# Performance work log

Measured on AMD Instinct MI355X. Metric: run time of the kernel, lower is better.

The kernel has to match this reference:

```python
import jax, jax.numpy as jnp
import numpy as np
from jax.scipy.linalg import expm

N_SPINS = 7
DIM = 2 ** N_SPINS  # 128
DT = 1e-05
B0 = 80.0
T2 = 1.0
PHASE = 0.0
SW = 1000.0


def _spin_ops():
    # Build per-spin angular-momentum operators via Kronecker embedding.
    sx = np.array([[0, 1], [1, 0]], dtype=np.complex64) / 2
    sy = np.array([[0, -1j], [1j, 0]], dtype=np.complex64) / 2
    sz = np.array([[1, 0], [0, -1]], dtype=np.complex64) / 2

    def embed(s):
        ops = []
        for i in range(N_SPINS):
            left = np.eye(2 ** i) if i > 0 else np.array(1.0)
            right = np.eye(2 ** (N_SPINS - i - 1)) if N_SPINS - i - 1 > 0 else np.array(1.0)
            ops.append(np.kron(np.kron(left, s), right))
        return np.stack(ops).astype(np.complex64)  # [n_spins, dim, dim]

    return embed(sx), embed(sy), embed(sz)


_IX, _IY, _IZ = _spin_ops()


def setup_inputs() -> dict:
    key = jax.random.key(0)
    h_mat = jax.random.normal(key, (N_SPINS, N_SPINS), dtype=jnp.float32)
    return {"h_mat": h_mat, "n_samp": 4096}


def reference(h_mat, n_samp):
    Ix = jnp.asarray(_IX)  # [n, d, d]
    Iy = jnp.asarray(_IY)
    Iz = jnpp_asarray = jnp.asarray(_IZ)
    Iz = jnp.asarray(_IZ)

    IHy = Iy.sum(axis=0)
    IHz = Iz.sum(axis=0)
    Op = Ix.sum(axis=0) + 1j * IHy  # IHx + i IHy

    hc = h_mat.astype(jnp.complex64)
    two_pi = 2.0 * jnp.pi

    # Pairwise two-spin couplings: C[i,j] = Ix_i Ix_j + Iy_i Iy_j + Iz_i Iz_j
    pair = (jnp.einsum('iab,jbc->ijac', Ix, Ix)
            + jnp.einsum('iab,jbc->ijac', Iy, Iy)
            + jnp.einsum('iab,jbc->ijac', Iz, Iz))
    upper = jnp.triu(jnp.ones((N_SPINS, N_SPINS), dtype=jnp.complex64), k=1)

    H0 = (two_pi * B0 * jnp.einsum('i,iab->ab', jnp.diagonal(hc), Iz)
          + two_pi * jnp.einsum('ij,ijac->ac', hc * upper, pair))

    # 90y pulse, then free evolution propagator
    U90y = expm(-1j * (jnp.pi / 2) * IHy)
    rho0 = U90y @ IHz @ U90y.conj().T
    P = expm(-1j * H0 * DT)
    Pd = P.conj().T

    def step(rho, _):
        tr = jnp.einsum('ij,ji->', Op, rho)  # trace(Op @ rho)
        return P @ rho @ Pd, tr

    _, traces = jax.lax.scan(step, rho0, None, length=n_samp)

    apod = jnp.exp((-DT / T2) * jnp.arange(n_samp, dtype=jnp.float32))
    FID = traces * apod.astype(jnp.complex64)

    spec = jnp.fft.fftshift(jnp.fft.fft(FID, 2 * n_samp))
    FTspec = jnp.exp(jnp.complex64(1j * PHASE)) * spec

    AQ = n_samp / SW
    time_series = jnp.linspace(0.0, AQ, n_samp, dtype=jnp.float32)
    freq_series = jnp.linspace(-SW / 2, SW / 2, 2 * n_samp, dtype=jnp.float32)
    return FID, time_series, FTspec, freq_series
```

## Files before the change

### kernel.cpp

```cpp
#include <hip/hip_runtime.h>
#include <math.h>

#define N_SAMP 4096
#define NS     7
#define DT_F   1e-5f
#define B0_F   80.0f
#define T2_F   1.0f
#define SW_F   1000.0f
#define TWO_PI 6.2831853071795864769f
#define EIG_T  640


__global__ __launch_bounds__(EIG_T) void k_eig(const float* __restrict__ h,
                                               float* __restrict__ Vc,
                                               float* __restrict__ Uc,
                                               float* __restrict__ lam_out) {
    const int nsz_[8]   = {1, 7, 21, 35, 35, 21, 7, 1};
    const int nbase_[8] = {0, 1, 8, 29, 64, 99, 120, 127};
    const int cum2_[8]  = {0, 1, 50, 491, 1716, 2941, 3382, 3431};
    const int offsU_[8] = {0, 0, 7, 154, 889, 2114, 2849, 2996};
    const int s    = blockIdx.x;
    const int ns   = nsz_[s];
    const int base = nbase_[s];
    const int tid  = threadIdx.x;
    const int wave = tid >> 6;
    const int lane = tid & 63;

    __shared__ float As[36 * 37];
    __shared__ float Vs[36 * 37];
    __shared__ int   st[36];
    __shared__ int   stm1[36];
    __shared__ int   inv[128];
    __shared__ float hs[49];
    __shared__ int   ppt2[21 * 12];
    __shared__ int   cnt2[21];

    const int ksm1 = (s >= 1) ? nsz_[s - 1] : 0;

    if (tid < 49) hs[tid] = h[tid];
    if (tid < 21) cnt2[tid] = 0;
    if (tid == 0) {
        int cnt = 0;
        for (int r = 0; r < 128; ++r) if (__popc(r) == s) st[cnt++] = r;
    }
    if (tid == 1 && s >= 1) {
        int cnt = 0;
        for (int r = 0; r < 128; ++r) if (__popc(r) == s - 1) stm1[cnt++] = r;
    }
    if (tid < 128 && __popc(tid) == s) {
        int cnt = 0;
        for (int r = 0; r < 128; ++r) { if (r == tid) break; if (__popc(r) == s) ++cnt; }
        inv[tid] = cnt;
    }
    for (int t = tid; t < 36 * 37; t += EIG_T) { As[t] = 0.f; Vs[t] = 0.f; }
    __syncthreads();

    if (ns > 1) {
        const int off_[7] = {0, 6, 11, 15, 18, 20, 0};
        for (int r = tid; r < 128; r += EIG_T) {
            if (__popc(r) == s) {
                for (int i = 0; i < 6; ++i) {
                    if (!((r >> i) & 1)) continue;
                    for (int j = i + 1; j < 7; ++j) {
                        if ((r >> j) & 1) continue;
                        int rid = off_[i] + (j - i - 1);
                        int prt = r ^ ((1 << i) | (1 << j));
                        int slot = atomicAdd(&cnt2[rid], 1);
                        ppt2[rid * 12 + slot] = (inv[r] << 8) | inv[prt];
                    }
                }
            }
        }
    }

    for (int t = tid; t < ns * ns; t += EIG_T) {
        int i = t / ns, j = t % ns;
        int r = st[i], c = st[j];
        float val = 0.f;
        if (r == c) {
            float acc = 0.f;
            for (int a = 0; a < 7; ++a) {
                float za = ((r >> (6 - a)) & 1) ? -0.5f : 0.5f;
                acc += B0_F * hs[a * 7 + a] * za;
                for (int b = a + 1; b < 7; ++b) {
                    float zb = ((r >> (6 - b)) & 1) ? -0.5f : 0.5f;
                    acc += hs[a * 7 + b] * za * zb;
                }
            }
            val = TWO_PI * acc;
        } else {
            int x = r ^ c;
            if (__popc(x) == 2) {
                int u = 31 - __clz(x);
                int v = __ffs(x) - 1;
                if (((r >> u) & 1) != ((r >> v) & 1))
                    val = TWO_PI * 0.5f * hs[(6 - u) * 7 + (6 - v)];
            }
        }
        As[i * 37 + j] = val;
    }
    for (int i = tid; i < ns; i += EIG_T) Vs[i * 37 + i] = 1.f;
    __syncthreads();

    if (ns > 1) {
        for (int t = 0; t < 21; ++t) {
            int npr = cnt2[t];
            float c0 = 1.f, s0 = 0.f;
            int   pq0 = -1;
            if (wave < npr) {
                int pq = ppt2[t * 12 + wave];
                int p = pq >> 8, q = pq & 255;
                float app = As[p * 37 + p];
                float aqq = As[q * 37 + q];
                float apq = As[p * 37 + q];
                float c = 1.f, sn = 0.f;
                if (fabsf(apq) >= 1e-30f) {
                    float tau = (aqq - app) / (2.f * apq);
                    float tt  = copysignf(1.f / (fabsf(tau) + sqrtf(1.f + tau * tau)), tau);
                    c  = rsqrtf(1.f + tt * tt);
                    sn = tt * c;
                }
                c0 = c; s0 = sn; pq0 = pq;
                if (lane < ns) {
                    float ap = As[p * 37 + lane], aq = As[q * 37 + lane];
                    As[p * 37 + lane] = c * ap - sn * aq;
                    As[q * 37 + lane] = sn * ap + c * aq;
                    float vp = Vs[p * 37 + lane], vq = Vs[q * 37 + lane];
                    Vs[p * 37 + lane] = c * vp - sn * vq;
                    Vs[q * 37 + lane] = sn * vp + c * vq;
                }
            }
            __syncthreads();
            if (pq0 >= 0) {
                int p = pq0 >> 8, q = pq0 & 255;
                if (lane < ns) {
                    float ap = As[lane * 37 + p], aq = As[lane * 37 + q];
                    As[lane * 37 + p] = c0 * ap - s0 * aq;
                    As[lane * 37 + q] = s0 * ap + c0 * aq;
                }
            }
            __syncthreads();
        }
    }

    for (int i = tid; i < ns; i += EIG_T) lam_out[base + i] = As[i * 37 + i];
    for (int t = tid; t < ns * ns; t += EIG_T) {
        int a = t / ns, k = t - (t / ns) * ns;
        Vc[cum2_[s] + t] = Vs[a * 37 + k];
    }
    if (s >= 1) {
        for (int t = tid; t < ns * ksm1; t += EIG_T) {
            int a = t / ksm1, i = t - (t / ksm1) * ksm1;
            int rr = stm1[i];
            float uval = 0.f;
#pragma unroll
            for (int p = 0; p < 7; ++p)
                if (!((rr >> p) & 1)) uval += Vs[a * 37 + inv[rr + (1 << p)]];
            Uc[offsU_[s] + t] = uval;
        }
    }
}

__global__ __launch_bounds__(128) void k_mwc(const float* __restrict__ Vc,
                                             const float* __restrict__ Uc,
                                             float* __restrict__ wc,
                                             int* __restrict__ ab) {
    const int n1_[7]   = {1, 7, 21, 35, 35, 21, 7};
    const int n2_[7]   = {7, 21, 35, 35, 21, 7, 1};
    const int offs_[7] = {0, 7, 154, 889, 2114, 2849, 2996};
    const int nb1_[7]  = {0, 1, 8, 29, 64, 99, 120};
    const int nb2_[7]  = {1, 8, 29, 64, 99, 120, 127};
    const int cum2_[7] = {0, 1, 50, 491, 1716, 2941, 3382};
    int e = blockIdx.x * 128 + threadIdx.x;
    if (e >= 3072) return;
    if (e >= 3003) { wc[e] = 0.f; ab[e] = 0; return; }
    int t = 0;
#pragma unroll
    for (int u = 1; u < 7; ++u) if (e >= offs_[u]) t = u;
    int loc = e - offs_[t];
    int n1 = n1_[t], n2 = n2_[t];
    int i = loc / n2;
    int j = loc - i * n2;
    const float* va = &Vc[cum2_[t] + i * n1];
    const float* ub = &Uc[offs_[t] + j * n1];
    float acc = 0.f;
    for (int k = 0; k < n1; ++k) acc += va[k] * ub[k];
    wc[e] = 0.5f * acc * acc;
    ab[e] = ((nb1_[t] + i) << 7) | (nb2_[t] + j);
}

__global__ __launch_bounds__(256) void k_fid(const float* __restrict__ wc,
                                             const int* __restrict__ ab,
                                             const float* __restrict__ lam,
                                             float* __restrict__ fidfF,
                                             float* __restrict__ out) {
    __shared__ float2 cb0[128], dd[128];
    __shared__ float  lred[4][16];
    const int n0  = blockIdx.x * 8;
    const int tid = threadIdx.x;
    const float t0 = (float)n0 * DT_F;
    if (tid < 128) {
        float sn, cs;
        sincosf(lam[tid] * t0, &sn, &cs);
        cb0[tid] = make_float2(cs, -sn);
        sincosf(lam[tid] * DT_F, &sn, &cs);
        dd[tid] = make_float2(cs, -sn);
    }
    __syncthreads();

    float ar0=0,ar1=0,ar2=0,ar3=0,ar4=0,ar5=0,ar6=0,ar7=0;
    float ai0=0,ai1=0,ai2=0,ai3=0,ai4=0,ai5=0,ai6=0,ai7=0;
#pragma unroll 4
    for (int i = 0; i < 12; ++i) {
        int e = i * 256 + tid;
        float w = wc[e];
        int pq = ab[e];
        int a = pq >> 7, b = pq & 127;
        float2 ca = cb0[a], cbv = cb0[b];
        float2 da = dd[a],  db  = dd[b];
        float zr = ca.x * cbv.x + ca.y * cbv.y;
        float zi = ca.x * cbv.y - ca.y * cbv.x;
        float fr = da.x * db.x + da.y * db.y;
        float fi = da.x * db.y - da.y * db.x;
        ar0 += w * zr; ai0 += w * zi; { float tr = zr*fr - zi*fi; zi = zr*fi + zi*fr; zr = tr; }
        ar1 += w * zr; ai1 += w * zi; { float tr = zr*fr - zi*fi; zi = zr*fi + zi*fr; zr = tr; }
        ar2 += w * zr; ai2 += w * zi; { float tr = zr*fr - zi*fi; zi = zr*fi + zi*fr; zr = tr; }
        ar3 += w * zr; ai3 += w * zi; { float tr = zr*fr - zi*fi; zi = zr*fi + zi*fr; zr = tr; }
        ar4 += w * zr; ai4 += w * zi; { float tr = zr*fr - zi*fi; zi = zr*fi + zi*fr; zr = tr; }
        ar5 += w * zr; ai5 += w * zi; { float tr = zr*fr - zi*fi; zi = zr*fi + zi*fr; zr = tr; }
        ar6 += w * zr; ai6 += w * zi; { float tr = zr*fr - zi*fi; zi = zr*fi + zi*fr; zr = tr; }
        ar7 += w * zr; ai7 += w * zi;
    }

    const int wave = tid >> 6, lane = tid & 63;
    float acc[16] = {ar0,ai0,ar1,ai1,ar2,ai2,ar3,ai3,ar4,ai4,ar5,ai5,ar6,ai6,ar7,ai7};
#pragma unroll 16
    for (int v = 0; v < 16; ++v) {
        float x = acc[v];
        for (int off = 32; off > 0; off >>= 1) x += __shfl_down(x, off);
        if (lane == 0) lred[wave][v] = x;
    }
    __syncthreads();
    if (tid < 16) {
        float x = lred[0][tid] + lred[1][tid] + lred[2][tid] + lred[3][tid];
        int jj = tid >> 1, c = tid & 1;
        int n = n0 + jj;
        float ap = expf(-(DT_F / T2_F) * (float)n);
        x *= ap;
        fidfF[2 * n + c] = x;
        if (c == 0) out[n] = x;
    }
}

__global__ __launch_bounds__(256) void k_dft(const float2* __restrict__ fidf,
                                             float* __restrict__ part) {
    __shared__ float2 fs[256];
    const int tid = threadIdx.x;
    const int ch  = blockIdx.x >> 5;
    const int kb  = blockIdx.x & 31;
    const int n0  = ch * 256;
    fs[tid] = fidf[n0 + tid];
    __syncthreads();
    const int k = kb * 256 + tid;
    const int K = (k + 4096) & 8191;
    const float C = TWO_PI / 8192.0f;
    int idx = (n0 * K) & 8191;
    float ar = 0.f;
    for (int i = 0; i < 256; ++i) {
        float2 s = fs[i];
        float sn, cs;
        __sincosf(C * (float)idx, &sn, &cs);
        ar += s.x * cs + s.y * sn;
        idx = (idx + K) & 8191;
    }
    part[ch * 8192 + k] = ar;
}

__global__ void k_dredax(const float* __restrict__ part, float* __restrict__ out) {
    int i = blockIdx.x * 256 + threadIdx.x;
    float s = 0.f;
#pragma unroll
    for (int ch = 0; ch < 16; ++ch) s += part[ch * 8192 + i];
    out[8192 + i] = s;
    out[16384 + i] = -0.5f * SW_F + (float)i * (SW_F / (float)(2 * N_SAMP - 1));
    if (i < N_SAMP)
        out[4096 + i] = (float)i * ((N_SAMP / SW_F) / (float)(N_SAMP - 1));
}

extern "C" void kernel_launch(void* const* d_in, const int* in_sizes, int n_in,
                              void* d_out, int out_size, void* d_ws, size_t ws_size,
                              hipStream_t stream) {
    const float* h = (const float*)d_in[0];
    float* out = (float*)d_out;
    float* ws  = (float*)d_ws;

    float*  Vc   = ws;
    float*  Uc   = ws + 4096;
    float*  lam  = ws + 16384;
    float*  wc   = ws + 49280;
    int*    ab   = (int*)(ws + 52352);
    float*  fidfF= ws + 65664;
    float2* fidf = (float2*)(ws + 65664);
    float*  part = ws + 73856;

    k_eig<<<8, EIG_T, 0, stream>>>(h, Vc, Uc, lam);
    k_mwc<<<24, 128, 0, stream>>>(Vc, Uc, wc, ab);
    k_fid<<<512, 256, 0, stream>>>(wc, ab, lam, fidfF, out);
    k_dft<<<512, 256, 0, stream>>>(fidf, part);
    k_dredax<<<32, 256, 0, stream>>>(part, out);
}
```

Measured before the change: 61.97 us.

## Compute spectrum analytically from eigen-transitions instead of DFT of FID

Replaces the two-stage DFT over the sampled FID (partial sums plus a reduction kernel) with a closed-form geometric-series sum over the ~3000 transition weights for each frequency bin. k_mwc now also precomputes each transition's half-phase step and its decayed end-phase factor, and k_spec evaluates the complex ratio per bin from shared memory. This removes the FID-to-spectrum dependency and one kernel launch, and cuts the per-bin work from 4096 samples to 3003 transitions. In exchange it relies on a hardcoded apodization constant and per-term divisions that may lose precision near resonances.

Result: slower. 101.7 us (+64.1%).

```diff
diff --git a/kernel.cpp b/kernel.cpp
--- a/kernel.cpp
+++ b/kernel.cpp
@@ -163,8 +163,12 @@
 
 __global__ __launch_bounds__(128) void k_mwc(const float* __restrict__ Vc,
                                              const float* __restrict__ Uc,
+                                             const float* __restrict__ lam,
                                              float* __restrict__ wc,
-                                             int* __restrict__ ab) {
+                                             int* __restrict__ ab,
+                                             float* __restrict__ hl,
+                                             float* __restrict__ sr,
+                                             float* __restrict__ si) {
     const int n1_[7]   = {1, 7, 21, 35, 35, 21, 7};
     const int n2_[7]   = {7, 21, 35, 35, 21, 7, 1};
     const int offs_[7] = {0, 7, 154, 889, 2114, 2849, 2996};
@@ -173,7 +177,7 @@
     const int cum2_[7] = {0, 1, 50, 491, 1716, 2941, 3382};
     int e = blockIdx.x * 128 + threadIdx.x;
     if (e >= 3072) return;
-    if (e >= 3003) { wc[e] = 0.f; ab[e] = 0; return; }
+    if (e >= 3003) { wc[e] = 0.f; ab[e] = 0; hl[e] = 0.f; sr[e] = 0.f; si[e] = 0.f; return; }
     int t = 0;
 #pragma unroll
     for (int u = 1; u < 7; ++u) if (e >= offs_[u]) t = u;
@@ -185,14 +189,22 @@
     const float* ub = &Uc[offs_[t] + j * n1];
     float acc = 0.f;
     for (int k = 0; k < n1; ++k) acc += va[k] * ub[k];
+    int a = nb1_[t] + i, b = nb2_[t] + j;
     wc[e] = 0.5f * acc * acc;
-    ab[e] = ((nb1_[t] + i) << 7) | (nb2_[t] + j);
+    ab[e] = (a << 7) | b;
+    float dl = lam[a] - lam[b];
+    hl[e] = dl * (DT_F * 0.5f);
+    const float TT = (float)N_SAMP * DT_F;
+    const float E  = expf(-TT / T2_F);
+    float s2, c2;
+    sincosf(dl * TT, &s2, &c2);
+    sr[e] = E * c2;
+    si[e] = E * s2;
 }
 
 __global__ __launch_bounds__(256) void k_fid(const float* __restrict__ wc,
                                              const int* __restrict__ ab,
                                              const float* __restrict__ lam,
-                                             float* __restrict__ fidfF,
                                              float* __restrict__ out) {
     __shared__ float2 cb0[128], dd[128];
     __shared__ float  lred[4][16];
@@ -247,44 +259,49 @@
         int n = n0 + jj;
         float ap = expf(-(DT_F / T2_F) * (float)n);
         x *= ap;
-        fidfF[2 * n + c] = x;
         if (c == 0) out[n] = x;
     }
 }
 
-__global__ __launch_bounds__(256) void k_dft(const float2* __restrict__ fidf,
-                                             float* __restrict__ part) {
-    __shared__ float2 fs[256];
+__global__ __launch_bounds__(256) void k_spec(const float* __restrict__ wc,
+                                              const float* __restrict__ hl,
+                                              const float* __restrict__ sr,
+                                              const float* __restrict__ si,
+                                              float* __restrict__ out) {
+    __shared__ float lwc[3072], lhl[3072], lsr[3072], lsi[3072];
     const int tid = threadIdx.x;
-    const int ch  = blockIdx.x >> 5;
-    const int kb  = blockIdx.x & 31;
-    const int n0  = ch * 256;
-    fs[tid] = fidf[n0 + tid];
-    __syncthreads();
-    const int k = kb * 256 + tid;
-    const int K = (k + 4096) & 8191;
-    const float C = TWO_PI / 8192.0f;
-    int idx = (n0 * K) & 8191;
-    float ar = 0.f;
-    for (int i = 0; i < 256; ++i) {
-        float2 s = fs[i];
-        float sn, cs;
-        __sincosf(C * (float)idx, &sn, &cs);
-        ar += s.x * cs + s.y * sn;
-        idx = (idx + K) & 8191;
-    }
-    part[ch * 8192 + k] = ar;
-}
-
-__global__ void k_dredax(const float* __restrict__ part, float* __restrict__ out) {
-    int i = blockIdx.x * 256 + threadIdx.x;
-    float s = 0.f;
+    for (int e = tid; e < 3072; e += 256) {
+        lwc[e] = wc[e]; lhl[e] = hl[e]; lsr[e] = sr[e]; lsi[e] = si[e];
+    }
+    __syncthreads();
+    const int kk = blockIdx.x * 32 + (tid >> 3);
+    const int l8 = tid & 7;
+    const int K  = (kk + 4096) & 8191;
+    const float pk  = (3.14159265358979f / 8192.0f) * (float)K;
+    const float skf = (K & 1) ? -1.f : 1.f;
+    const float A = 9.99995000e-06f;
+    const float B = 0.99999000005f;
+    float acc = 0.f;
+    for (int e = l8; e < 3072; e += 8) {
+        float ph = lhl[e] - pk;
+        float sh, ch;
+        __sincosf(ph, &sh, &ch);
+        float dr = A + 2.f * B * sh * sh;
+        float di = -2.f * B * sh * ch;
+        float nr = 1.f - skf * lsr[e];
+        float ni = -skf * lsi[e];
+        float num = nr * dr + ni * di;
+        float den = dr * dr + di * di;
+        acc += lwc[e] * num / den;
+    }
 #pragma unroll
-    for (int ch = 0; ch < 16; ++ch) s += part[ch * 8192 + i];
-    out[8192 + i] = s;
-    out[16384 + i] = -0.5f * SW_F + (float)i * (SW_F / (float)(2 * N_SAMP - 1));
-    if (i < N_SAMP)
-        out[4096 + i] = (float)i * ((N_SAMP / SW_F) / (float)(N_SAMP - 1));
+    for (int off = 4; off > 0; off >>= 1) acc += __shfl_down(acc, off, 8);
+    if (l8 == 0) {
+        out[8192 + kk] = acc;
+        out[16384 + kk] = -0.5f * SW_F + (float)kk * (SW_F / (float)(2 * N_SAMP - 1));
+        if (kk < N_SAMP)
+            out[4096 + kk] = (float)kk * ((N_SAMP / SW_F) / (float)(N_SAMP - 1));
+    }
 }
 
 extern "C" void kernel_launch(void* const* d_in, const int* in_sizes, int n_in,
@@ -299,13 +316,12 @@
     float*  lam  = ws + 16384;
     float*  wc   = ws + 49280;
     int*    ab   = (int*)(ws + 52352);
-    float*  fidfF= ws + 65664;
-    float2* fidf = (float2*)(ws + 65664);
-    float*  part = ws + 73856;
+    float*  hl   = ws + 55424;
+    float*  sr   = ws + 58496;
+    float*  si   = ws + 61568;
 
     k_eig<<<8, EIG_T, 0, stream>>>(h, Vc, Uc, lam);
-    k_mwc<<<24, 128, 0, stream>>>(Vc, Uc, wc, ab);
-    k_fid<<<512, 256, 0, stream>>>(wc, ab, lam, fidfF, out);
-    k_dft<<<512, 256, 0, stream>>>(fidf, part);
-    k_dredax<<<32, 256, 0, stream>>>(part, out);
-}
+    k_mwc<<<24, 128, 0, stream>>>(Vc, Uc, lam, wc, ab, hl, sr, si);
+    k_fid<<<512, 256, 0, stream>>>(wc, ab, lam, out);
+    k_spec<<<256, 256, 0, stream>>>(wc, hl, sr, si, out);
+}
```

## Fuse DFT reduction via atomics and replace per-sample sincos with rotation recurrence

Applied to the files above, without the earlier changes.

Drops the separate reduction kernel. k_dft now atomically adds its partial sums straight into the spectrum output, which k_mwc zeroes in advance along with the time and frequency axes. Inside the DFT loop, the per-iteration __sincosf is replaced by a complex-rotation recurrence that starts from one initial sincos. This removes a kernel launch, the partial-sum buffer traffic and most transcendental calls. In exchange it adds atomic contention across 16 chunks, makes the summation order nondeterministic, and lets rounding error build up over 256 recurrence steps.

Result: faster. 57.27 us (-7.6%).

```diff
diff --git a/kernel.cpp b/kernel.cpp
--- a/kernel.cpp
+++ b/kernel.cpp
@@ -164,7 +164,8 @@
 __global__ __launch_bounds__(128) void k_mwc(const float* __restrict__ Vc,
                                              const float* __restrict__ Uc,
                                              float* __restrict__ wc,
-                                             int* __restrict__ ab) {
+                                             int* __restrict__ ab,
+                                             float* __restrict__ out) {
     const int n1_[7]   = {1, 7, 21, 35, 35, 21, 7};
     const int n2_[7]   = {7, 21, 35, 35, 21, 7, 1};
     const int offs_[7] = {0, 7, 154, 889, 2114, 2849, 2996};
@@ -172,6 +173,14 @@
     const int nb2_[7]  = {1, 8, 29, 64, 99, 120, 127};
     const int cum2_[7] = {0, 1, 50, 491, 1716, 2941, 3382};
     int e = blockIdx.x * 128 + threadIdx.x;
+
+    for (int i = e; i < 8192; i += 3072) {
+        out[8192 + i] = 0.f;
+        out[16384 + i] = -0.5f * SW_F + (float)i * (SW_F / (float)(2 * N_SAMP - 1));
+        if (i < N_SAMP)
+            out[4096 + i] = (float)i * ((N_SAMP / SW_F) / (float)(N_SAMP - 1));
+    }
+
     if (e >= 3072) return;
     if (e >= 3003) { wc[e] = 0.f; ab[e] = 0; return; }
     int t = 0;
@@ -253,38 +262,29 @@
 }
 
 __global__ __launch_bounds__(256) void k_dft(const float2* __restrict__ fidf,
-                                             float* __restrict__ part) {
-    __shared__ float2 fs[256];
+                                             float* __restrict__ out) {
+    __shared__ float2 fsh[256];
     const int tid = threadIdx.x;
     const int ch  = blockIdx.x >> 5;
     const int kb  = blockIdx.x & 31;
     const int n0  = ch * 256;
-    fs[tid] = fidf[n0 + tid];
+    fsh[tid] = fidf[n0 + tid];
     __syncthreads();
     const int k = kb * 256 + tid;
     const int K = (k + 4096) & 8191;
     const float C = TWO_PI / 8192.0f;
-    int idx = (n0 * K) & 8191;
+    float zs, zc, fs_, fc;
+    __sincosf(C * (float)((n0 * K) & 8191), &zs, &zc);
+    __sincosf(C * (float)K, &fs_, &fc);
     float ar = 0.f;
     for (int i = 0; i < 256; ++i) {
-        float2 s = fs[i];
-        float sn, cs;
-        __sincosf(C * (float)idx, &sn, &cs);
-        ar += s.x * cs + s.y * sn;
-        idx = (idx + K) & 8191;
-    }
-    part[ch * 8192 + k] = ar;
-}
-
-__global__ void k_dredax(const float* __restrict__ part, float* __restrict__ out) {
-    int i = blockIdx.x * 256 + threadIdx.x;
-    float s = 0.f;
-#pragma unroll
-    for (int ch = 0; ch < 16; ++ch) s += part[ch * 8192 + i];
-    out[8192 + i] = s;
-    out[16384 + i] = -0.5f * SW_F + (float)i * (SW_F / (float)(2 * N_SAMP - 1));
-    if (i < N_SAMP)
-        out[4096 + i] = (float)i * ((N_SAMP / SW_F) / (float)(N_SAMP - 1));
+        float2 s = fsh[i];
+        ar += s.x * zc + s.y * zs;
+        float t = zc * fc - zs * fs_;
+        zs = zc * fs_ + zs * fc;
+        zc = t;
+    }
+    atomicAdd(&out[8192 + k], ar);
 }
 
 extern "C" void kernel_launch(void* const* d_in, const int* in_sizes, int n_in,
@@ -301,11 +301,9 @@
     int*    ab   = (int*)(ws + 52352);
     float*  fidfF= ws + 65664;
     float2* fidf = (float2*)(ws + 65664);
-    float*  part = ws + 73856;
 
     k_eig<<<8, EIG_T, 0, stream>>>(h, Vc, Uc, lam);
-    k_mwc<<<24, 128, 0, stream>>>(Vc, Uc, wc, ab);
+    k_mwc<<<24, 128, 0, stream>>>(Vc, Uc, wc, ab, out);
     k_fid<<<512, 256, 0, stream>>>(wc, ab, lam, fidfF, out);
-    k_dft<<<512, 256, 0, stream>>>(fidf, part);
-    k_dredax<<<32, 256, 0, stream>>>(part, out);
-}
+    k_dft<<<512, 256, 0, stream>>>(fidf, out);
+}
```
